# Kernel tuning notes

Hardware: AMD Instinct MI355X
Metric: run time of the kernel (lower is better)

The kernel has to match this reference:

```python
import jax, jax.numpy as jnp
import numpy as np

N = 50000       # nodes
E = 800000      # edges (avg degree 16)
C_IN = 128
C_OUT = 128
H = 4           # attention heads
D = C_OUT // H  # per-head dim
G = 8           # group-norm groups
NEG_SLOPE_ACT = 0.01   # nn.LeakyReLU() default
NEG_SLOPE_ATT = 0.2    # GAT attention LeakyReLU slope


def _glorot(key, shape):
    fan = shape[0] + (shape[-1] if len(shape) > 1 else shape[0])
    lim = np.sqrt(6.0 / fan).astype(np.float32)
    return jax.random.uniform(key, shape, jnp.float32, -lim, lim)


def setup_inputs() -> dict:
    key = jax.random.key(0)
    ks = jax.random.split(key, 8)
    inp = {
        "x": jax.random.normal(ks[0], (N, C_IN), jnp.float32),
        "edge_index": jax.random.randint(ks[1], (2, E), 0, N),
        "edge_weight": jax.random.uniform(ks[2], (E,), jnp.float32),
    }
    dims = [C_IN, C_OUT]
    for l in range(2):
        cin = dims[l]
        k = jax.random.split(ks[3 + l], 8)
        inp[f"gamma{l}"] = jnp.ones((cin,), jnp.float32)
        inp[f"beta{l}"] = jnp.zeros((cin,), jnp.float32)
        inp[f"W{l}"] = _glorot(k[0], (cin, H * D))
        inp[f"We{l}"] = _glorot(k[1], (1, H * D))
        inp[f"a_src{l}"] = _glorot(k[2], (H, D))
        inp[f"a_dst{l}"] = _glorot(k[3], (H, D))
        inp[f"a_edge{l}"] = _glorot(k[4], (H, D))
        inp[f"bias{l}"] = jnp.zeros((H * D,), jnp.float32)
    return inp


def group_norm(x, gamma, beta, eps=1e-5):
    n, c = x.shape
    xg = x.reshape(n, G, c // G)
    mu = xg.mean(-1, keepdims=True)
    var = xg.var(-1, keepdims=True)
    xn = ((xg - mu) * jax.lax.rsqrt(var + eps)).reshape(n, c)
    return xn * gamma + beta


def gat_layer(x, src, dst, ew, W, We, a_src, a_dst, a_edge, bias):
    h = (x @ W).reshape(N, H, D)                   # [N,H,D]
    he = (ew[:, None] @ We).reshape(-1, H, D)      # [E',H,D] edge-weight embedding
    logits = ((h * a_src).sum(-1)[src]
              + (h * a_dst).sum(-1)[dst]
              + (he * a_edge).sum(-1))             # [E',H]
    logits = jax.nn.leaky_relu(logits, NEG_SLOPE_ATT)
    m = jax.ops.segment_max(logits, dst, num_segments=N)
    m = jax.lax.stop_gradient(jnp.where(jnp.isfinite(m), m, 0.0))
    e = jnp.exp(logits - m[dst])
    s = jax.ops.segment_sum(e, dst, num_segments=N)
    alpha = e / (s[dst] + 1e-16)                   # softmax over in-edges per dst, per head
    out = jax.ops.segment_sum(alpha[:, :, None] * h[src], dst, num_segments=N)
    return out.reshape(N, H * D) + bias


def reference(x, edge_index, edge_weight,
              gamma0, beta0, W0, We0, a_src0, a_dst0, a_edge0, bias0,
              gamma1, beta1, W1, We1, a_src1, a_dst1, a_edge1, bias1):
    loop = jnp.arange(N)
    src = jnp.concatenate([edge_index[0], loop])
    dst = jnp.concatenate([edge_index[1], loop])
    # self-loop fill_value='max': self edges get the max edge weight
    ew = jnp.concatenate([edge_weight, jnp.full((N,), edge_weight.max())])
    params = [(gamma0, beta0, W0, We0, a_src0, a_dst0, a_edge0, bias0),
              (gamma1, beta1, W1, We1, a_src1, a_dst1, a_edge1, bias1)]
    for g, b, W, We, asrc, adst, ae, bias in params:
        x = group_norm(x, g, b)
        x = jax.nn.leaky_relu(x, NEG_SLOPE_ACT)
        x = gat_layer(x, src, dst, ew, W, We, asrc, adst, ae, bias)
    return x
```

## Files before the change

### kernel.cpp

```cpp
#include <hip/hip_runtime.h>
#include <hip/hip_bf16.h>
#include <math.h>

#define CN 128
#define NBLK 256
#define BSH 8

typedef __attribute__((ext_vector_type(8))) short bf16x8;
typedef __attribute__((ext_vector_type(4))) float f32x4;

static __device__ inline unsigned int pack_bf16x2(float lo, float hi) {
    unsigned int ul = __float_as_uint(lo);
    unsigned int uh = __float_as_uint(hi);
    ul = (ul + 0x7fffu + ((ul >> 16) & 1u)) >> 16;
    uh = (uh + 0x7fffu + ((uh >> 16) & 1u)) & 0xffff0000u;
    return ul | uh;
}
static __device__ inline unsigned short bf16_of(float v) {
    unsigned int u = __float_as_uint(v);
    return (unsigned short)((u + 0x7fffu + ((u >> 16) & 1u)) >> 16);
}

__global__ __launch_bounds__(256) void kbA(const int* __restrict__ dsts,
                                           const float* __restrict__ ew,
                                           int e, int n,
                                           int* __restrict__ hist,
                                           int* __restrict__ ewmaxArr,
                                           const float* __restrict__ W0,
                                           const float* __restrict__ W1,
                                           const float* __restrict__ We0,
                                           const float* __restrict__ ae0,
                                           const float* __restrict__ We1,
                                           const float* __restrict__ ae1,
                                           unsigned short* __restrict__ wt0,
                                           unsigned short* __restrict__ wt1,
                                           float* __restrict__ ce) {
    __shared__ int lh[256];
    __shared__ int wm[4];
    int t = threadIdx.x, blk = blockIdx.x;
    if (blk >= NBLK) {
        int b = blk - NBLK;
        if (b < 2) {
            const float* W = b ? W1 : W0;
            unsigned short* wt = b ? wt1 : wt0;
            for (int i = t; i < CN * CN; i += 256) {
                int k = i >> 7, c = i & 127;
                wt[c * CN + k] = bf16_of(W[k * CN + c]);
            }
        } else if (t < 8) {
            const float* We = (t < 4) ? We0 : We1;
            const float* ae = (t < 4) ? ae0 : ae1;
            int h = t & 3;
            float s = 0.f;
            for (int d = 0; d < 32; d++) s += We[h * 32 + d] * ae[h * 32 + d];
            ce[t] = s;
        }
        return;
    }
    lh[t] = 0;
    __syncthreads();
    int tot = e + n;
    int chunk = (tot + NBLK - 1) / NBLK;
    int start = blk * chunk, end = min(start + chunk, tot);
    float m = 0.f;
    for (int i = start + t; i < end; i += 256) {
        int d;
        if (i < e) { d = dsts[i]; m = fmaxf(m, ew[i]); }
        else       { d = i - e; }
        atomicAdd(&lh[d >> BSH], 1);
    }
#pragma unroll
    for (int off = 1; off < 64; off <<= 1) m = fmaxf(m, __shfl_xor(m, off));
    if ((t & 63) == 0) wm[t >> 6] = __float_as_int(m);
    __syncthreads();
    hist[t * NBLK + blk] = lh[t];
    if (t == 0)
        ewmaxArr[blk] = max(max(wm[0], wm[1]), max(wm[2], wm[3]));
}

__global__ __launch_bounds__(256) void kscanL(int* __restrict__ a,
                                              int* __restrict__ bsum) {
    __shared__ int wsum[4];
    int t = threadIdx.x, blk = blockIdx.x;
    int idx = blk * 256 + t;
    int v = a[idx];
    int s = v;
    int lane = t & 63, wid = t >> 6;
#pragma unroll
    for (int off = 1; off < 64; off <<= 1) {
        int u = __shfl_up(s, off);
        if (lane >= off) s += u;
    }
    if (lane == 63) wsum[wid] = s;
    __syncthreads();
    int add = 0;
#pragma unroll
    for (int w = 0; w < 4; w++) if (w < wid) add += wsum[w];
    s += add;
    a[idx] = s - v;
    if (t == 255) bsum[blk] = s;
}

__global__ __launch_bounds__(256) void kbB(const int* __restrict__ srcs,
                                           const int* __restrict__ dsts,
                                           const float* __restrict__ ew,
                                           const int* __restrict__ ewmaxArr,
                                           const int* __restrict__ hsc,
                                           const int* __restrict__ bsum,
                                           int2* __restrict__ inter, int e, int n) {
    __shared__ int cur[256];
    __shared__ int wsum[4];
    __shared__ int wmI;
    int t = threadIdx.x, blk = blockIdx.x;
    if (t == 0) wmI = 0;
    int v = bsum[t];
    int s = v;
    int lane = t & 63, wid = t >> 6;
#pragma unroll
    for (int off = 1; off < 64; off <<= 1) {
        int u = __shfl_up(s, off);
        if (lane >= off) s += u;
    }
    int mi = ewmaxArr[t];
#pragma unroll
    for (int off = 1; off < 64; off <<= 1) mi = max(mi, __shfl_xor(mi, off));
    if (lane == 63) wsum[wid] = s;
    __syncthreads();
    int add = 0;
#pragma unroll
    for (int w = 0; w < 4; w++) if (w < wid) add += wsum[w];
    s += add;
    cur[t] = hsc[t * NBLK + blk] + (s - v);
    if (lane == 0) atomicMax(&wmI, mi);
    __syncthreads();
    float wmax = __int_as_float(wmI);
    int tot = e + n;
    int chunk = (tot + NBLK - 1) / NBLK;
    int start = blk * chunk, end = min(start + chunk, tot);
    for (int i = start + t; i < end; i += 256) {
        int sn, d; float w;
        if (i < e) { sn = srcs[i]; d = dsts[i]; w = ew[i]; }
        else       { sn = i - e;   d = sn;      w = wmax;  }
        int p = atomicAdd(&cur[d >> BSH], 1);
        inter[p] = make_int2((d << 16) | sn, __float_as_int(w));
    }
}

__global__ __launch_bounds__(256) void kbC(const int* __restrict__ hsc,
                                           const int* __restrict__ bsum,
                                           const int2* __restrict__ inter,
                                           unsigned int* __restrict__ edges,
                                           int* __restrict__ rowptr,
                                           int n, int nb, int ep) {
    __shared__ int cnt[256];
    __shared__ int cur[256];
    __shared__ int wsum[4];
    __shared__ int bexc[257];
    int t = threadIdx.x, b = blockIdx.x;
    int lane = t & 63, wid = t >> 6;
    {
        int v = bsum[t];
        int s = v;
#pragma unroll
        for (int off = 1; off < 64; off <<= 1) {
            int u = __shfl_up(s, off);
            if (lane >= off) s += u;
        }
        if (lane == 63) wsum[wid] = s;
        __syncthreads();
        int add = 0;
#pragma unroll
        for (int w = 0; w < 4; w++) if (w < wid) add += wsum[w];
        s += add;
        bexc[t] = s - v;
        if (t == 255) bexc[256] = s;
    }
    cnt[t] = 0;
    __syncthreads();
    int rstart = hsc[b * NBLK] + bexc[b];
    int rend = (b + 1 < 256) ? (hsc[(b + 1) * NBLK] + bexc[b + 1]) : ep;
    for (int i = rstart + t; i < rend; i += 256)
        atomicAdd(&cnt[(inter[i].x >> 16) & 255], 1);
    __syncthreads();
    int v = cnt[t];
    int s = v;
#pragma unroll
    for (int off = 1; off < 64; off <<= 1) {
        int u = __shfl_up(s, off);
        if (lane >= off) s += u;
    }
    if (lane == 63) wsum[wid] = s;
    __syncthreads();
    int wexcl = 0;
#pragma unroll
    for (int w = 0; w < 4; w++) if (w < wid) wexcl += wsum[w];
    int excl = wexcl + s - v;
    int node = (b << BSH) + t;
    int gpos = rstart + excl;
    if (node < n) rowptr[node] = gpos;
    if (b == nb - 1 && t == 0) rowptr[n] = ep;
    cur[t] = gpos;
    __syncthreads();
    for (int i = rstart + t; i < rend; i += 256) {
        int2 r = inter[i];
        int p = atomicAdd(&cur[(r.x >> 16) & 255], 1);
        unsigned int wb = bf16_of(__int_as_float(r.y));
        edges[p] = (unsigned int)(r.x & 0xffff) | (wb << 16);
    }
}

__global__ __launch_bounds__(256, 3) void kgn_gemm7(
        const float* __restrict__ xin, const uint4* __restrict__ xin_b,
        int inbf16, const float* __restrict__ gamma,
        const float* __restrict__ beta, const unsigned short* __restrict__ wt,
        const float* __restrict__ asrc, const float* __restrict__ adst,
        unsigned int* __restrict__ hout, float* __restrict__ ssrc,
        float* __restrict__ sdst, int n) {
    __shared__ short xs[64 * CN];
    __shared__ short ws[CN * CN];

    int t = threadIdx.x;
    int lane = t & 63, w = t >> 6;
    int m = lane & 15, quad = lane >> 4;
    int block_row = blockIdx.x * 64;

    {
        const uint4* src = (const uint4*)wt;
        uint4* dst = (uint4*)ws;
#pragma unroll
        for (int i = 0; i < 8; i++) {
            int u = t + 256 * i;
            int c = u >> 4, kb = u & 15;
            dst[c * 16 + (kb ^ (c & 15))] = src[u];
        }
    }
    {
        int r = t & 63;
        int row = block_row + r;
        uint4* dst = (uint4*)xs;
#pragma unroll
        for (int u2 = 0; u2 < 2; u2++) {
            int g = (t >> 6) * 2 + u2;
            uint4 lo, hi;
            if (row < n) {
                float v[16];
                if (inbf16) {
                    uint4 A = xin_b[(size_t)row * 16 + g * 2];
                    uint4 B = xin_b[(size_t)row * 16 + g * 2 + 1];
                    unsigned int uu[8] = {A.x,A.y,A.z,A.w,B.x,B.y,B.z,B.w};
#pragma unroll
                    for (int j = 0; j < 8; j++) {
                        v[2*j]   = __uint_as_float(uu[j] << 16);
                        v[2*j+1] = __uint_as_float(uu[j] & 0xffff0000u);
                    }
                } else {
                    const float4* xr = (const float4*)(xin + (size_t)row * CN + g * 16);
                    float4 A = xr[0], B = xr[1], C = xr[2], D = xr[3];
                    float tmp[16] = {A.x,A.y,A.z,A.w,B.x,B.y,B.z,B.w,
                                     C.x,C.y,C.z,C.w,D.x,D.y,D.z,D.w};
#pragma unroll
                    for (int j = 0; j < 16; j++) v[j] = tmp[j];
                }
                float mu = 0.f;
#pragma unroll
                for (int j = 0; j < 16; j++) mu += v[j];
                mu *= 0.0625f;
                float var = 0.f;
#pragma unroll
                for (int j = 0; j < 16; j++) { float d2 = v[j] - mu; var += d2 * d2; }
                var *= 0.0625f;
                float rsv = rsqrtf(var + 1e-5f);
                const float4* gp = (const float4*)(gamma + g * 16);
                const float4* bp = (const float4*)(beta + g * 16);
                float4 g0 = gp[0], g1 = gp[1], g2 = gp[2], g3 = gp[3];
                float4 b0 = bp[0], b1 = bp[1], b2 = bp[2], b3 = bp[3];
                float gv[16] = {g0.x,g0.y,g0.z,g0.w,g1.x,g1.y,g1.z,g1.w,
                                g2.x,g2.y,g2.z,g2.w,g3.x,g3.y,g3.z,g3.w};
                float bv[16] = {b0.x,b0.y,b0.z,b0.w,b1.x,b1.y,b1.z,b1.w,
                                b2.x,b2.y,b2.z,b2.w,b3.x,b3.y,b3.z,b3.w};
                float xn[16];
#pragma unroll
                for (int j = 0; j < 16; j++) {
                    float xv = (v[j] - mu) * rsv * gv[j] + bv[j];
                    xn[j] = xv > 0.f ? xv : 0.01f * xv;
                }
                lo = make_uint4(pack_bf16x2(xn[0], xn[1]),  pack_bf16x2(xn[2], xn[3]),
                                pack_bf16x2(xn[4], xn[5]),  pack_bf16x2(xn[6], xn[7]));
                hi = make_uint4(pack_bf16x2(xn[8], xn[9]),  pack_bf16x2(xn[10], xn[11]),
                                pack_bf16x2(xn[12], xn[13]), pack_bf16x2(xn[14], xn[15]));
            } else {
                lo = make_uint4(0, 0, 0, 0);
                hi = lo;
            }
            dst[r * 16 + ((2 * g)     ^ (r & 15))] = lo;
            dst[r * 16 + ((2 * g + 1) ^ (r & 15))] = hi;
        }
    }
    __syncthreads();

    f32x4 acc[4][2];
#pragma unroll
    for (int i = 0; i < 4; i++) { acc[i][0] = (f32x4)0.f; acc[i][1] = (f32x4)0.f; }

#pragma unroll
    for (int kc = 0; kc < 4; kc++) {
        int kb = 4 * kc + quad;
        bf16x8 af[4], bfr[2];
#pragma unroll
        for (int mt = 0; mt < 4; mt++)
            af[mt] = *(const bf16x8*)&xs[(16 * mt + m) * CN + ((kb ^ m) << 3)];
#pragma unroll
        for (int nt = 0; nt < 2; nt++) {
            int c = 32 * w + 16 * nt + m;
            bfr[nt] = *(const bf16x8*)&ws[c * CN + ((kb ^ m) << 3)];
        }
#pragma unroll
        for (int mt = 0; mt < 4; mt++) {
#pragma unroll
            for (int nt = 0; nt < 2; nt++)
                acc[mt][nt] = __builtin_amdgcn_mfma_f32_16x16x32_bf16(
                    af[mt], bfr[nt], acc[mt][nt], 0, 0, 0);
        }
    }

    float asv[2], adv[2];
#pragma unroll
    for (int nt = 0; nt < 2; nt++) {
        asv[nt] = asrc[32 * w + 16 * nt + m];
        adv[nt] = adst[32 * w + 16 * nt + m];
    }
#pragma unroll
    for (int mt = 0; mt < 4; mt++) {
#pragma unroll
        for (int j = 0; j < 4; j++) {
            float p = acc[mt][0][j] * asv[0] + acc[mt][1][j] * asv[1];
            float q = acc[mt][0][j] * adv[0] + acc[mt][1][j] * adv[1];
#pragma unroll
            for (int off = 1; off < 16; off <<= 1) {
                p += __shfl_xor(p, off);
                q += __shfl_xor(q, off);
            }
            if (m == 0) {
                int row = block_row + 16 * mt + 4 * quad + j;
                if (row < n) {
                    ssrc[row * 4 + w] = p;
                    sdst[row * 4 + w] = q;
                }
            }
        }
    }

    __syncthreads();
#pragma unroll
    for (int mt = 0; mt < 4; mt++) {
#pragma unroll
        for (int nt = 0; nt < 2; nt++) {
            int c = 32 * w + 16 * nt + m;
#pragma unroll
            for (int j = 0; j < 4; j++) {
                int rl = 16 * mt + 4 * quad + j;
                xs[rl * CN + c] = (short)bf16_of(acc[mt][nt][j]);
            }
        }
    }
    __syncthreads();
    {
        const uint4* src = (const uint4*)xs;
#pragma unroll
        for (int i = 0; i < 4; i++) {
            int u = t + 256 * i;
            int rl = u >> 4;
            int row = block_row + rl;
            if (row < n)
                *(uint4*)&hout[(size_t)row * 64 + ((u & 15) << 2)] = src[u];
        }
    }
}

__global__ __launch_bounds__(256, 8) void kaggr3(
        const uint4* __restrict__ h, const float* __restrict__ ssrc,
        const float* __restrict__ sdst, const int* __restrict__ rowptr,
        const unsigned int* __restrict__ edges, const float* __restrict__ ce4,
        const float* __restrict__ bias, float* __restrict__ out,
        uint4* __restrict__ outb, int packout, int n) {
    int t = threadIdx.x;
    int node = blockIdx.x * 4 + (t >> 6);
    if (node >= n) return;
    int l64 = t & 63;
    int ll = l64 & 15;
    int g  = l64 >> 4;
    int head = ll >> 2;

    int start = rowptr[node], end = rowptr[node + 1];
    float sd = sdst[node * 4 + head];
    float ce = ce4[head];

    float a0=0.f,a1=0.f,a2=0.f,a3=0.f,a4=0.f,a5=0.f,a6=0.f,a7=0.f;
    float se = 0.f;

    int i = start + g;
    for (; i + 12 < end; i += 16) {
        unsigned int er[4];
#pragma unroll
        for (int u = 0; u < 4; u++) er[u] = edges[i + 4 * u];
        float ssv[4]; uint4 U[4];
#pragma unroll
        for (int u = 0; u < 4; u++) {
            int sidx = er[u] & 0xffff;
            ssv[u] = ssrc[sidx * 4 + head];
            U[u] = h[(size_t)sidx * 16 + ll];
        }
#pragma unroll
        for (int u = 0; u < 4; u++) {
            float wv = __uint_as_float(er[u] & 0xffff0000u);
            float l = ssv[u] + sd + wv * ce;
            l = fmaxf(l, 0.2f * l);
            float e = __expf(fminf(l, 80.f));
            float h0 = __uint_as_float(U[u].x << 16);
            float h1 = __uint_as_float(U[u].x & 0xffff0000u);
            float h2 = __uint_as_float(U[u].y << 16);
            float h3 = __uint_as_float(U[u].y & 0xffff0000u);
            float h4 = __uint_as_float(U[u].z << 16);
            float h5 = __uint_as_float(U[u].z & 0xffff0000u);
            float h6 = __uint_as_float(U[u].w << 16);
            float h7 = __uint_as_float(U[u].w & 0xffff0000u);
            se += e;
            a0 = fmaf(e, h0, a0); a1 = fmaf(e, h1, a1);
            a2 = fmaf(e, h2, a2); a3 = fmaf(e, h3, a3);
            a4 = fmaf(e, h4, a4); a5 = fmaf(e, h5, a5);
            a6 = fmaf(e, h6, a6); a7 = fmaf(e, h7, a7);
        }
    }
    for (; i < end; i += 4) {
        unsigned int er = edges[i];
        int sidx = er & 0xffff;
        float ss = ssrc[sidx * 4 + head];
        uint4 U = h[(size_t)sidx * 16 + ll];
        float wv = __uint_as_float(er & 0xffff0000u);
        float l = ss + sd + wv * ce;
        l = fmaxf(l, 0.2f * l);
        float e = __expf(fminf(l, 80.f));
        float h0 = __uint_as_float(U.x << 16);
        float h1 = __uint_as_float(U.x & 0xffff0000u);
        float h2 = __uint_as_float(U.y << 16);
        float h3 = __uint_as_float(U.y & 0xffff0000u);
        float h4 = __uint_as_float(U.z << 16);
        float h5 = __uint_as_float(U.z & 0xffff0000u);
        float h6 = __uint_as_float(U.w << 16);
        float h7 = __uint_as_float(U.w & 0xffff0000u);
        se += e;
        a0 = fmaf(e, h0, a0); a1 = fmaf(e, h1, a1);
        a2 = fmaf(e, h2, a2); a3 = fmaf(e, h3, a3);
        a4 = fmaf(e, h4, a4); a5 = fmaf(e, h5, a5);
        a6 = fmaf(e, h6, a6); a7 = fmaf(e, h7, a7);
    }
#pragma unroll
    for (int off = 16; off < 64; off <<= 1) {
        a0 += __shfl_xor(a0, off); a1 += __shfl_xor(a1, off);
        a2 += __shfl_xor(a2, off); a3 += __shfl_xor(a3, off);
        a4 += __shfl_xor(a4, off); a5 += __shfl_xor(a5, off);
        a6 += __shfl_xor(a6, off); a7 += __shfl_xor(a7, off);
        se += __shfl_xor(se, off);
    }
    if (g == 0) {
        float inv = 1.f / (se + 1e-16f);
        const float4* bp = (const float4*)(bias + ll * 8);
        float4 b0 = bp[0], b1 = bp[1];
        float o0 = a0 * inv + b0.x, o1 = a1 * inv + b0.y;
        float o2 = a2 * inv + b0.z, o3 = a3 * inv + b0.w;
        float o4 = a4 * inv + b1.x, o5 = a5 * inv + b1.y;
        float o6 = a6 * inv + b1.z, o7 = a7 * inv + b1.w;
        if (packout) {
            outb[(size_t)node * 16 + ll] =
                make_uint4(pack_bf16x2(o0, o1), pack_bf16x2(o2, o3),
                           pack_bf16x2(o4, o5), pack_bf16x2(o6, o7));
        } else {
            float4* orow = (float4*)(out + (size_t)node * CN + ll * 8);
            orow[0] = make_float4(o0, o1, o2, o3);
            orow[1] = make_float4(o4, o5, o6, o7);
        }
    }
}

extern "C" void kernel_launch(void* const* d_in, const int* in_sizes, int n_in,
                              void* d_out, int out_size, void* d_ws, size_t ws_size,
                              hipStream_t stream) {
    const float* x  = (const float*)d_in[0];
    const int*   ei = (const int*)d_in[1];
    const float* ew = (const float*)d_in[2];
    int N_ = in_sizes[0] / CN;
    int E_ = in_sizes[2];
    int EP = E_ + N_;
    int NB = (N_ + 255) >> BSH;

    size_t off = 0;
    auto alloc = [&](size_t bytes) -> void* {
        void* p = (char*)d_ws + off;
        off += (bytes + 255) & ~(size_t)255;
        return p;
    };
    unsigned int* hbuf = (unsigned int*)alloc((size_t)N_ * 64 * 4);
    uint4* x1b     = (uint4*)alloc((size_t)N_ * 64 * 4);
    float* ssrc    = (float*)alloc((size_t)N_ * 4 * 4);
    float* sdst    = (float*)alloc((size_t)N_ * 4 * 4);
    int*   rowptr  = (int*)alloc((size_t)(N_ + 1) * 4);
    unsigned int* edges = (unsigned int*)alloc((size_t)EP * 4);
    int2*  inter   = (int2*)alloc((size_t)EP * 8);
    int*   hist    = (int*)alloc((size_t)256 * NBLK * 4);
    int*   bsum    = (int*)alloc(1024);
    int*   ewmaxArr= (int*)alloc((size_t)NBLK * 4);
    unsigned short* wt0 = (unsigned short*)alloc((size_t)CN * CN * 2);
    unsigned short* wt1 = (unsigned short*)alloc((size_t)CN * CN * 2);
    float* cedge   = (float*)alloc(256);

    const int* srcs = ei;
    const int* dsts = ei + E_;

    kbA<<<NBLK + 3, 256, 0, stream>>>(dsts, ew, E_, N_, hist, ewmaxArr,
                                      (const float*)d_in[5], (const float*)d_in[13],
                                      (const float*)d_in[6], (const float*)d_in[9],
                                      (const float*)d_in[14], (const float*)d_in[17],
                                      wt0, wt1, cedge);
    kscanL<<<256, 256, 0, stream>>>(hist, bsum);
    kbB<<<NBLK, 256, 0, stream>>>(srcs, dsts, ew, ewmaxArr, hist, bsum, inter, E_, N_);
    kbC<<<NB, 256, 0, stream>>>(hist, bsum, inter, edges, rowptr, N_, NB, EP);

    for (int l = 0; l < 2; l++) {
        const float* gamma = (const float*)d_in[3 + l * 8 + 0];
        const float* beta  = (const float*)d_in[3 + l * 8 + 1];
        const float* asrc  = (const float*)d_in[3 + l * 8 + 4];
        const float* adst  = (const float*)d_in[3 + l * 8 + 5];
        const float* bias  = (const float*)d_in[3 + l * 8 + 7];
        const unsigned short* wt = (l == 0) ? wt0 : wt1;

        kgn_gemm7<<<(N_ + 63) / 64, 256, 0, stream>>>(
            x, (const uint4*)x1b, l, gamma, beta, wt, asrc, adst,
            hbuf, ssrc, sdst, N_);
        kaggr3<<<(N_ + 3) / 4, 256, 0, stream>>>(
            (const uint4*)hbuf, ssrc, sdst, rowptr, edges, cedge + l * 4,
            bias, (float*)d_out, x1b, (l == 0) ? 1 : 0, N_);
    }
}
```

Baseline: 260.3 us.

## Merge CSR scatter kernel with layer-0 GroupNorm+GEMM into one launch

```diff
diff --git a/kernel.cpp b/kernel.cpp
--- a/kernel.cpp
+++ b/kernel.cpp
@@ -146,17 +146,15 @@
     }
 }
 
-__global__ __launch_bounds__(256) void kbC(const int* __restrict__ hsc,
-                                           const int* __restrict__ bsum,
-                                           const int2* __restrict__ inter,
-                                           unsigned int* __restrict__ edges,
-                                           int* __restrict__ rowptr,
-                                           int n, int nb, int ep) {
-    __shared__ int cnt[256];
-    __shared__ int cur[256];
-    __shared__ int wsum[4];
-    __shared__ int bexc[257];
-    int t = threadIdx.x, b = blockIdx.x;
+static __device__ void kbc_body(int* cnt, int* cur, int* wsum, int* bexc,
+                                int b,
+                                const int* __restrict__ hsc,
+                                const int* __restrict__ bsum,
+                                const int2* __restrict__ inter,
+                                unsigned int* __restrict__ edges,
+                                int* __restrict__ rowptr,
+                                int n, int nb, int ep) {
+    int t = threadIdx.x;
     int lane = t & 63, wid = t >> 6;
     {
         int v = bsum[t];
@@ -209,20 +207,20 @@
     }
 }
 
-__global__ __launch_bounds__(256, 3) void kgn_gemm7(
-        const float* __restrict__ xin, const uint4* __restrict__ xin_b,
-        int inbf16, const float* __restrict__ gamma,
-        const float* __restrict__ beta, const unsigned short* __restrict__ wt,
-        const float* __restrict__ asrc, const float* __restrict__ adst,
-        unsigned int* __restrict__ hout, float* __restrict__ ssrc,
-        float* __restrict__ sdst, int n) {
-    __shared__ short xs[64 * CN];
-    __shared__ short ws[CN * CN];
-
+static __device__ void kgn_body(short* xs, short* ws, int block_row,
+                                const float* __restrict__ xin,
+                                const uint4* __restrict__ xin_b,
+                                int inbf16, const float* __restrict__ gamma,
+                                const float* __restrict__ beta,
+                                const unsigned short* __restrict__ wt,
+                                const float* __restrict__ asrc,
+                                const float* __restrict__ adst,
+                                unsigned int* __restrict__ hout,
+                                float* __restrict__ ssrc,
+                                float* __restrict__ sdst, int n) {
     int t = threadIdx.x;
     int lane = t & 63, w = t >> 6;
     int m = lane & 15, quad = lane >> 4;
-    int block_row = blockIdx.x * 64;
 
     {
         const uint4* src = (const uint4*)wt;
@@ -375,6 +373,43 @@
                 *(uint4*)&hout[(size_t)row * 64 + ((u & 15) << 2)] = src[u];
         }
     }
+}
+
+__global__ __launch_bounds__(256, 3) void kbCgn(
+        const int* __restrict__ hsc, const int* __restrict__ bsum,
+        const int2* __restrict__ inter, unsigned int* __restrict__ edges,
+        int* __restrict__ rowptr, int n, int nb, int ep,
+        const float* __restrict__ xin, const float* __restrict__ gamma,
+        const float* __restrict__ beta, const unsigned short* __restrict__ wt,
+        const float* __restrict__ asrc, const float* __restrict__ adst,
+        unsigned int* __restrict__ hout, float* __restrict__ ssrcO,
+        float* __restrict__ sdstO) {
+    __shared__ short xs[64 * CN];
+    __shared__ short ws[CN * CN];
+    if ((int)blockIdx.x < nb) {
+        int* cnt  = (int*)xs;
+        int* cur  = (int*)(xs + 512);
+        int* wsum = (int*)(xs + 1024);
+        int* bexc = (int*)(xs + 2048);
+        kbc_body(cnt, cur, wsum, bexc, blockIdx.x,
+                 hsc, bsum, inter, edges, rowptr, n, nb, ep);
+        return;
+    }
+    kgn_body(xs, ws, ((int)blockIdx.x - nb) * 64, xin, (const uint4*)0, 0,
+             gamma, beta, wt, asrc, adst, hout, ssrcO, sdstO, n);
+}
+
+__global__ __launch_bounds__(256, 3) void kgn_gemm7(
+        const float* __restrict__ xin, const uint4* __restrict__ xin_b,
+        int inbf16, const float* __restrict__ gamma,
+        const float* __restrict__ beta, const unsigned short* __restrict__ wt,
+        const float* __restrict__ asrc, const float* __restrict__ adst,
+        unsigned int* __restrict__ hout, float* __restrict__ ssrc,
+        float* __restrict__ sdst, int n) {
+    __shared__ short xs[64 * CN];
+    __shared__ short ws[CN * CN];
+    kgn_body(xs, ws, blockIdx.x * 64, xin, xin_b, inbf16,
+             gamma, beta, wt, asrc, adst, hout, ssrc, sdst, n);
 }
 
 __global__ __launch_bounds__(256, 8) void kaggr3(
@@ -492,6 +527,7 @@
     int E_ = in_sizes[2];
     int EP = E_ + N_;
     int NB = (N_ + 255) >> BSH;
+    int NT = (N_ + 63) / 64;
 
     size_t off = 0;
     auto alloc = [&](size_t bytes) -> void* {
@@ -523,21 +559,22 @@
                                       wt0, wt1, cedge);
     kscanL<<<256, 256, 0, stream>>>(hist, bsum);
     kbB<<<NBLK, 256, 0, stream>>>(srcs, dsts, ew, ewmaxArr, hist, bsum, inter, E_, N_);
-    kbC<<<NB, 256, 0, stream>>>(hist, bsum, inter, edges, rowptr, N_, NB, EP);
-
-    for (int l = 0; l < 2; l++) {
-        const float* gamma = (const float*)d_in[3 + l * 8 + 0];
-        const float* beta  = (const float*)d_in[3 + l * 8 + 1];
-        const float* asrc  = (const float*)d_in[3 + l * 8 + 4];
-        const float* adst  = (const float*)d_in[3 + l * 8 + 5];
-        const float* bias  = (const float*)d_in[3 + l * 8 + 7];
-        const unsigned short* wt = (l == 0) ? wt0 : wt1;
-
-        kgn_gemm7<<<(N_ + 63) / 64, 256, 0, stream>>>(
-            x, (const uint4*)x1b, l, gamma, beta, wt, asrc, adst,
-            hbuf, ssrc, sdst, N_);
-        kaggr3<<<(N_ + 3) / 4, 256, 0, stream>>>(
-            (const uint4*)hbuf, ssrc, sdst, rowptr, edges, cedge + l * 4,
-            bias, (float*)d_out, x1b, (l == 0) ? 1 : 0, N_);
-    }
-}
+
+    kbCgn<<<NB + NT, 256, 0, stream>>>(
+        hist, bsum, inter, edges, rowptr, N_, NB, EP,
+        x, (const float*)d_in[3], (const float*)d_in[4], wt0,
+        (const float*)d_in[7], (const float*)d_in[8],
+        hbuf, ssrc, sdst);
+
+    kaggr3<<<(N_ + 3) / 4, 256, 0, stream>>>(
+        (const uint4*)hbuf, ssrc, sdst, rowptr, edges, cedge,
+        (const float*)d_in[10], (float*)d_out, x1b, 1, N_);
+
+    kgn_gemm7<<<NT, 256, 0, stream>>>(
+        x, (const uint4*)x1b, 1, (const float*)d_in[11], (const float*)d_in[12],
+        wt1, (const float*)d_in[15], (const float*)d_in[16],
+        hbuf, ssrc, sdst, N_);
+    kaggr3<<<(N_ + 3) / 4, 256, 0, stream>>>(
+        (const uint4*)hbuf, ssrc, sdst, rowptr, edges, cedge + 4,
+        (const float*)d_in[18], (float*)d_out, x1b, 0, N_);
+}
```

Result: no change. 256.9 us (-1.3%).
